# Kernel tuning notes

Hardware: AMD Instinct MI355X
Metric: run time of the kernel (lower is better)

The kernel has to match this reference:

```python
import math
import jax, jax.numpy as jnp
import numpy as np

SM_K = 5

def make_sm_kernel(kernel_size=SM_K, sigma_e=1.2, sigma_i=1.4):
    center = kernel_size // 2
    xx, yy = jnp.meshgrid(jnp.arange(kernel_size, dtype=jnp.float32),
                          jnp.arange(kernel_size, dtype=jnp.float32), indexing='ij')
    xx = xx - center
    yy = yy - center
    g_e = jnp.exp(-(xx ** 2 + yy ** 2) / (2.0 * sigma_e ** 2))
    g_i = jnp.exp(-(xx ** 2 + yy ** 2) / (2.0 * sigma_i ** 2))
    dog = g_e / (2.0 * math.pi * sigma_e ** 2) - g_i / (2.0 * math.pi * sigma_i ** 2)
    return dog / dog[center, center]  # (5,5), normalized so center == 1


def setup_inputs() -> dict:
    key = jax.random.key(0)
    k1, k2 = jax.random.split(key)
    B, Cin, H, W = 16, 64, 128, 128
    Cout, K = 64, 5
    x = jax.random.normal(k1, (B, Cin, H, W), dtype=jnp.float32)
    weight_range = 25.0 / math.sqrt(Cin * K * K)
    weight = weight_range * jnp.abs(jax.random.normal(k2, (Cout, Cin, K, K), dtype=jnp.float32))
    return {"x": x, "weight": weight}


def reference(x, weight):
    PAD = 2
    dn = ('NCHW', 'OIHW', 'NCHW')
    Cout = weight.shape[0]
    K = weight.shape[-1]

    # symmetric_pad -> F.pad reflect
    xp = jnp.pad(x, ((0, 0), (0, 0), (PAD, PAD), (PAD, PAD)), mode='reflect')

    # w = weight.abs(); F.normalize(w, p=2, dim=1): L2 norm over in_channels per (o, kh, kw)
    w = jnp.abs(weight)
    nrm = jnp.sqrt(jnp.sum(w * w, axis=1, keepdims=True))
    w_n = w / jnp.maximum(nrm, 1e-12)

    # cosine similarity: conv with normalized weights / input patch norm
    conv = jax.lax.conv_general_dilated(xp, w_n, (1, 1), 'VALID', dimension_numbers=dn)
    # conv(x^2, ones_like(w)) yields identical values for every output channel;
    # compute once with a single-output-channel ones kernel and broadcast.
    ones_k = jnp.ones((1, x.shape[1], K, K), dtype=x.dtype)
    xsq_sum = jax.lax.conv_general_dilated(xp * xp, ones_k, (1, 1), 'VALID', dimension_numbers=dn)
    y = conv / jnp.sqrt(xsq_sum + 1e-8)  # (B, Cout, H, W)

    # surround modulation: depthwise conv with fixed 5x5 DoG kernel, padding 2
    sm = make_sm_kernel()
    sm_k = jnp.broadcast_to(sm[None, None].astype(y.dtype), (Cout, 1, SM_K, SM_K))
    y = jax.lax.conv_general_dilated(y, sm_k, (1, 1), [(SM_K // 2, SM_K // 2)] * 2,
                                     dimension_numbers=dn, feature_group_count=Cout)
    return y
```

## Files before the change

kernel.cpp:

```cpp
#include <hip/hip_runtime.h>
#include <hip/hip_bf16.h>
#include <math.h>

#define B_   16
#define CIN  64
#define COUT 64
#define H_   128
#define W_   128
#define KK   25
#define HW   (H_ * W_)
#define XT_PLANE ((size_t)B_ * HW * 32)

typedef short  bf16x8 __attribute__((ext_vector_type(8)));
typedef short  s16x4  __attribute__((ext_vector_type(4)));
typedef float  f32x16 __attribute__((ext_vector_type(16)));
typedef float  f32x4  __attribute__((ext_vector_type(4)));
typedef float  f32x2  __attribute__((ext_vector_type(2)));

__device__ __forceinline__ short f2bs(float v) {
    __hip_bfloat16 h = __float2bfloat16(v);
    return *reinterpret_cast<short*>(&h);
}
__device__ __forceinline__ float bs2f(short s) {
    unsigned int u = ((unsigned int)(unsigned short)s) << 16;
    return __uint_as_float(u);
}

__global__ __launch_bounds__(256) void k_prep(const float* __restrict__ x,
                                              const float* __restrict__ w,
                                              short* __restrict__ xt,
                                              float* __restrict__ xsqg,
                                              short* __restrict__ wnb2) {
    const int tid = threadIdx.x;

    if (blockIdx.z == B_) {
        if (blockIdx.x != 0 || blockIdx.y >= COUT) return;
        __shared__ float wl[CIN * KK];
        __shared__ float inv[KK];
        const int o = blockIdx.y;

        for (int idx = tid; idx < CIN * KK; idx += 256)
            wl[idx] = w[(size_t)o * (CIN * KK) + idx];
        __syncthreads();
        if (tid < KK) {
            float s = 0.f;
            #pragma unroll 8
            for (int i = 0; i < CIN; ++i) { float v = wl[i * KK + tid]; s += v * v; }
            inv[tid] = 1.f / fmaxf(sqrtf(s), 1e-12f);
        }
        __syncthreads();
        const int tt = o >> 5, n = o & 31;
        for (int idx = tid; idx < CIN * KK; idx += 256) {
            int ci = idx & 63, kk = idx >> 6;
            int ks = ci >> 4, q = (ci >> 3) & 1, j = ci & 7;
            int l = q * 32 + n;
            wnb2[((size_t)((kk * 4 + ks) * 2 + tt) * 64 + l) * 8 + j] =
                f2bs(fabsf(wl[ci * KK + kk]) * inv[kk]);
        }
        return;
    }

    __shared__ float tile[64][65];
    __shared__ float ps[4][64];
    const int b = blockIdx.z, h = blockIdx.y, w0 = blockIdx.x * 64;

    const float* xb = x + (size_t)b * CIN * HW + h * W_ + w0;
    {
        int wl = tid & 63, c0 = tid >> 6;
        float sq = 0.f;
        #pragma unroll
        for (int cc = 0; cc < 16; ++cc) {
            float v = xb[(size_t)(c0 * 16 + cc) * HW + wl];
            tile[c0 * 16 + cc][wl] = v;
            sq += v * v;
        }
        ps[c0][wl] = sq;
    }
    __syncthreads();

    const size_t pixbase = (size_t)b * HW + h * W_ + w0;
    if (tid < 64)
        xsqg[pixbase + tid] = ps[0][tid] + ps[1][tid] + ps[2][tid] + ps[3][tid];

    {
        int c8 = tid & 7;
        int half = c8 >> 2, sl = c8 & 3;
        short* dp = xt + (size_t)half * XT_PLANE;
        #pragma unroll
        for (int rep = 0; rep < 2; ++rep) {
            int p = (tid >> 3) + rep * 32;
            bf16x8 v;
            #pragma unroll
            for (int j = 0; j < 8; ++j) v[j] = f2bs(tile[c8 * 8 + j][p]);
            *(bf16x8*)&dp[(pixbase + p) * 32 + sl * 8] = v;
        }
    }
}

#define XP 40
#define NR 12
#define NC 36
#define NS (NR * NC)
#define TP 264

__global__ __launch_bounds__(256, 4) void k_conv(const short* __restrict__ xt,
                                                 const float* __restrict__ xsqg,
                                                 const short* __restrict__ wnb2,
                                                 __hip_bfloat16* __restrict__ t) {
    __shared__ short xin[NS * XP];
    __shared__ float s2win[NS];
    __shared__ int   soff[NS];
    __shared__ float xsq[256];

    const int tid  = threadIdx.x;
    const int lane = tid & 63;
    const int wv   = tid >> 6;
    const int n    = lane & 31;
    const int q    = lane >> 5;
    const int b    = blockIdx.z;
    const int h0   = blockIdx.y * 8;
    const int w0   = blockIdx.x * 32;

    const size_t pixbase = (size_t)b * HW;

    for (int s = tid; s < NS; s += 256) {
        int r = s / NC, c = s - r * NC;
        int hh = h0 - 2 + r; hh = hh < 0 ? -hh : (hh > H_ - 1 ? 2 * (H_ - 1) - hh : hh);
        int ww = w0 - 2 + c; ww = ww < 0 ? -ww : (ww > W_ - 1 ? 2 * (W_ - 1) - ww : ww);
        int off = hh * W_ + ww;
        soff[s] = off;
        s2win[s] = xsqg[pixbase + off];
    }
    __syncthreads();

    {
        int hr = tid >> 5, cl = tid & 31;
        float a = 0.f;
        #pragma unroll
        for (int kh = 0; kh < 5; ++kh)
            #pragma unroll
            for (int kw = 0; kw < 5; ++kw)
                a += s2win[(hr + kh) * NC + cl + kw];
        xsq[tid] = a;
    }

    const short* wb = wnb2 + (size_t)lane * 8;

    f32x16 acc00, acc01, acc10, acc11;
    #pragma unroll
    for (int i = 0; i < 16; ++i) { acc00[i] = 0.f; acc01[i] = 0.f; acc10[i] = 0.f; acc11[i] = 0.f; }

    #pragma unroll
    for (int half = 0; half < 2; ++half) {
        const short* xph = xt + (size_t)half * XT_PLANE + pixbase * 32;
        for (int i = tid; i < NS * 4; i += 256) {
            int s = i >> 2, c8 = i & 3;
            *(bf16x8*)&xin[s * 32 + c8 * 8 + (s * 8 & 2047) * 0 + s * (XP - 32)] =
                *(const bf16x8*)&xph[(size_t)soff[s] * 32 + c8 * 8];
        }
        __syncthreads();

        #pragma unroll 5
        for (int kk = 0; kk < KK; ++kk) {
            const int kh = kk / 5, kw = kk % 5;
            const int sp0 = (2 * wv + kh) * NC + n + kw;
            #pragma unroll
            for (int ks2 = 0; ks2 < 2; ++ks2) {
                const int ks = half * 2 + ks2;
                const int ko = ks2 * 16 + q * 8;
                bf16x8 a0 = *(const bf16x8*)&xin[sp0 * XP + ko];
                bf16x8 a1 = *(const bf16x8*)&xin[(sp0 + NC) * XP + ko];
                bf16x8 b0 = *(const bf16x8*)&wb[(size_t)((kk * 4 + ks) * 2 + 0) * 512];
                bf16x8 b1 = *(const bf16x8*)&wb[(size_t)((kk * 4 + ks) * 2 + 1) * 512];
                acc00 = __builtin_amdgcn_mfma_f32_32x32x16_bf16(a0, b0, acc00, 0, 0, 0);
                acc01 = __builtin_amdgcn_mfma_f32_32x32x16_bf16(a0, b1, acc01, 0, 0, 0);
                acc10 = __builtin_amdgcn_mfma_f32_32x32x16_bf16(a1, b0, acc10, 0, 0, 0);
                acc11 = __builtin_amdgcn_mfma_f32_32x32x16_bf16(a1, b1, acc11, 0, 0, 0);
            }
        }
        __syncthreads();
    }

    short* trans = xin;
    const int hrA = 2 * wv, hrB = 2 * wv + 1;
    #pragma unroll
    for (int g4 = 0; g4 < 4; ++g4) {
        int wc0 = 8 * g4 + 4 * q;
        s16x4 v00, v01, v10, v11;
        #pragma unroll
        for (int j = 0; j < 4; ++j) {
            float ia = rsqrtf(xsq[hrA * 32 + wc0 + j] + 1e-8f);
            float ib = rsqrtf(xsq[hrB * 32 + wc0 + j] + 1e-8f);
            v00[j] = f2bs(acc00[4 * g4 + j] * ia);
            v01[j] = f2bs(acc01[4 * g4 + j] * ia);
            v10[j] = f2bs(acc10[4 * g4 + j] * ib);
            v11[j] = f2bs(acc11[4 * g4 + j] * ib);
        }
        *(s16x4*)&trans[n * TP        + hrA * 32 + wc0] = v00;
        *(s16x4*)&trans[(32 + n) * TP + hrA * 32 + wc0] = v01;
        *(s16x4*)&trans[n * TP        + hrB * 32 + wc0] = v10;
        *(s16x4*)&trans[(32 + n) * TP + hrB * 32 + wc0] = v11;
    }
    __syncthreads();

    #pragma unroll
    for (int u = tid; u < 512; u += 256) {
        int oc = u >> 3, hr = u & 7;
        const short* src = &trans[oc * TP + hr * 32];
        __hip_bfloat16* dst = t + ((size_t)(b * COUT + oc) * H_ + h0 + hr) * W_ + w0;
        float4 a0 = *(const float4*)(src);
        float4 a1 = *(const float4*)(src + 8);
        float4 a2 = *(const float4*)(src + 16);
        float4 a3 = *(const float4*)(src + 24);
        *(float4*)(dst)      = a0;
        *(float4*)(dst + 8)  = a1;
        *(float4*)(dst + 16) = a2;
        *(float4*)(dst + 24) = a3;
    }
}

__global__ __launch_bounds__(256) void k_dog(const __hip_bfloat16* __restrict__ t,
                                             float* __restrict__ out) {
    __shared__ float tile[68 * 132];
    __shared__ float sm_s[25];
    const int bo  = blockIdx.y;
    const int h0  = blockIdx.x * 64;
    const int tid = threadIdx.x;

    if (tid < 25) {
        const float se2 = 2.f * 1.2f * 1.2f;
        const float si2 = 2.f * 1.4f * 1.4f;
        const float twopi = 6.28318530717958647692f;
        const float ae = 1.f / (twopi * 1.2f * 1.2f);
        const float ai = 1.f / (twopi * 1.4f * 1.4f);
        const float c0 = ae - ai;
        int dx = tid / 5 - 2, dy = tid % 5 - 2;
        float r2 = (float)(dx * dx + dy * dy);
        sm_s[tid] = (ae * expf(-r2 / se2) - ai * expf(-r2 / si2)) / c0;
    }

    const __hip_bfloat16* tc = t + (size_t)bo * HW;
    for (int idx = tid; idx < 68 * 16; idx += 256) {
        int rr = idx >> 4, g = idx & 15;
        int hh = h0 - 2 + rr;
        float v[8];
        if (hh >= 0 && hh < H_) {
            bf16x8 a = *(const bf16x8*)&tc[hh * W_ + g * 8];
            #pragma unroll
            for (int j = 0; j < 8; ++j) v[j] = bs2f(a[j]);
        } else {
            #pragma unroll
            for (int j = 0; j < 8; ++j) v[j] = 0.f;
        }
        float* dst = &tile[rr * 132 + 2 + g * 8];
        *(f32x2*)(dst)     = (f32x2){v[0], v[1]};
        *(f32x4*)(dst + 2) = (f32x4){v[2], v[3], v[4], v[5]};
        *(f32x2*)(dst + 6) = (f32x2){v[6], v[7]};
    }
    for (int idx = tid; idx < 68 * 4; idx += 256) {
        int rr = idx >> 2, c = idx & 3;
        tile[rr * 132 + (c < 2 ? c : 128 + c)] = 0.f;
    }
    __syncthreads();

    float smr[25];
    #pragma unroll
    for (int kk = 0; kk < 25; ++kk) smr[kk] = sm_s[kk];

    const int cq = tid & 31;
    const int r0 = tid >> 5;
    #pragma unroll
    for (int rr = 0; rr < 8; ++rr) {
        int r = r0 + 8 * rr;
        float s0 = 0.f, s1 = 0.f, s2 = 0.f, s3 = 0.f;
        #pragma unroll
        for (int kh = 0; kh < 5; ++kh) {
            const float* row = &tile[(r + kh) * 132 + cq * 4];
            f32x4 v0 = *(const f32x4*)(row);
            f32x4 v1 = *(const f32x4*)(row + 4);
            float vv[8] = { v0[0], v0[1], v0[2], v0[3], v1[0], v1[1], v1[2], v1[3] };
            #pragma unroll
            for (int kw = 0; kw < 5; ++kw) {
                float cf = smr[kh * 5 + kw];
                s0 += cf * vv[kw];
                s1 += cf * vv[kw + 1];
                s2 += cf * vv[kw + 2];
                s3 += cf * vv[kw + 3];
            }
        }
        float4 o4 = make_float4(s0, s1, s2, s3);
        *(float4*)&out[((size_t)bo * H_ + h0 + r) * W_ + cq * 4] = o4;
    }
}

extern "C" void kernel_launch(void* const* d_in, const int* in_sizes, int n_in,
                              void* d_out, int out_size, void* d_ws, size_t ws_size,
                              hipStream_t stream) {
    const float* x = (const float*)d_in[0];
    const float* w = (const float*)d_in[1];

    __hip_bfloat16* t = (__hip_bfloat16*)d_ws;

    short* xt    = (short*)d_out;
    float* xsqg  = (float*)((char*)d_out + 33554432);
    short* wnb2  = (short*)((char*)d_out + (size_t)67108864 - 204800);

    dim3 gx(W_ / 64, H_, B_ + 1);
    k_prep<<<gx, 256, 0, stream>>>(x, w, xt, xsqg, wnb2);

    dim3 g2(W_ / 32, H_ / 8, B_);
    k_conv<<<g2, 256, 0, stream>>>(xt, xsqg, wnb2, t);

    dim3 g3(H_ / 64, B_ * COUT);
    k_dog<<<g3, 256, 0, stream>>>(t, (float*)d_out);
}
```

Before: 190.8 us.

## Tile intermediate layout by width strip and vectorize prep input loads

Measured after the change: 189.9 us. Within noise of the previous version (-0.5%).

```diff
diff --git a/kernel.cpp b/kernel.cpp
--- a/kernel.cpp
+++ b/kernel.cpp
@@ -10,6 +10,7 @@
 #define KK   25
 #define HW   (H_ * W_)
 #define XT_PLANE ((size_t)B_ * HW * 32)
+#define WTS ((size_t)COUT * H_ * 32)
 
 typedef short  bf16x8 __attribute__((ext_vector_type(8)));
 typedef short  s16x4  __attribute__((ext_vector_type(4)));
@@ -61,27 +62,22 @@
     }
 
     __shared__ float tile[64][65];
-    __shared__ float ps[4][64];
+    __shared__ float ps[8][64];
     const int b = blockIdx.z, h = blockIdx.y, w0 = blockIdx.x * 64;
 
     const float* xb = x + (size_t)b * CIN * HW + h * W_ + w0;
     {
-        int wl = tid & 63, c0 = tid >> 6;
-        float sq = 0.f;
-        #pragma unroll
-        for (int cc = 0; cc < 16; ++cc) {
-            float v = xb[(size_t)(c0 * 16 + cc) * HW + wl];
-            tile[c0 * 16 + cc][wl] = v;
-            sq += v * v;
-        }
-        ps[c0][wl] = sq;
+        int c4 = tid & 15, g = tid >> 4;
+        #pragma unroll
+        for (int k = 0; k < 4; ++k) {
+            int ci = g * 4 + k;
+            *(f32x4*)&tile[ci][c4 * 4] =
+                *(const f32x4*)&xb[(size_t)ci * HW + c4 * 4];
+        }
     }
     __syncthreads();
 
     const size_t pixbase = (size_t)b * HW + h * W_ + w0;
-    if (tid < 64)
-        xsqg[pixbase + tid] = ps[0][tid] + ps[1][tid] + ps[2][tid] + ps[3][tid];
-
     {
         int c8 = tid & 7;
         int half = c8 >> 2, sl = c8 & 3;
@@ -89,11 +85,23 @@
         #pragma unroll
         for (int rep = 0; rep < 2; ++rep) {
             int p = (tid >> 3) + rep * 32;
-            bf16x8 v;
-            #pragma unroll
-            for (int j = 0; j < 8; ++j) v[j] = f2bs(tile[c8 * 8 + j][p]);
+            bf16x8 v; float sq = 0.f;
+            #pragma unroll
+            for (int j = 0; j < 8; ++j) {
+                float f = tile[c8 * 8 + j][p];
+                sq += f * f;
+                v[j] = f2bs(f);
+            }
+            ps[c8][p] = sq;
             *(bf16x8*)&dp[(pixbase + p) * 32 + sl * 8] = v;
         }
+    }
+    __syncthreads();
+    if (tid < 64) {
+        float a = 0.f;
+        #pragma unroll
+        for (int c8 = 0; c8 < 8; ++c8) a += ps[c8][tid];
+        xsqg[pixbase + tid] = a;
     }
 }
 
@@ -106,7 +114,7 @@
 __global__ __launch_bounds__(256, 4) void k_conv(const short* __restrict__ xt,
                                                  const float* __restrict__ xsqg,
                                                  const short* __restrict__ wnb2,
-                                                 __hip_bfloat16* __restrict__ t) {
+                                                 short* __restrict__ t2) {
     __shared__ short xin[NS * XP];
     __shared__ float s2win[NS];
     __shared__ int   soff[NS];
@@ -119,7 +127,8 @@
     const int q    = lane >> 5;
     const int b    = blockIdx.z;
     const int h0   = blockIdx.y * 8;
-    const int w0   = blockIdx.x * 32;
+    const int wt   = blockIdx.x;
+    const int w0   = wt * 32;
 
     const size_t pixbase = (size_t)b * HW;
 
@@ -155,7 +164,7 @@
         const short* xph = xt + (size_t)half * XT_PLANE + pixbase * 32;
         for (int i = tid; i < NS * 4; i += 256) {
             int s = i >> 2, c8 = i & 3;
-            *(bf16x8*)&xin[s * 32 + c8 * 8 + (s * 8 & 2047) * 0 + s * (XP - 32)] =
+            *(bf16x8*)&xin[s * XP + c8 * 8] =
                 *(const bf16x8*)&xph[(size_t)soff[s] * 32 + c8 * 8];
         }
         __syncthreads();
@@ -203,11 +212,12 @@
     }
     __syncthreads();
 
+    short* tbase = t2 + ((size_t)(b * 4 + wt) * COUT) * (H_ * 32);
     #pragma unroll
     for (int u = tid; u < 512; u += 256) {
         int oc = u >> 3, hr = u & 7;
         const short* src = &trans[oc * TP + hr * 32];
-        __hip_bfloat16* dst = t + ((size_t)(b * COUT + oc) * H_ + h0 + hr) * W_ + w0;
+        short* dst = tbase + ((size_t)oc * H_ + h0 + hr) * 32;
         float4 a0 = *(const float4*)(src);
         float4 a1 = *(const float4*)(src + 8);
         float4 a2 = *(const float4*)(src + 16);
@@ -219,7 +229,7 @@
     }
 }
 
-__global__ __launch_bounds__(256) void k_dog(const __hip_bfloat16* __restrict__ t,
+__global__ __launch_bounds__(256) void k_dog(const short* __restrict__ t2,
                                              float* __restrict__ out) {
     __shared__ float tile[68 * 132];
     __shared__ float sm_s[25];
@@ -239,13 +249,15 @@
         sm_s[tid] = (ae * expf(-r2 / se2) - ai * expf(-r2 / si2)) / c0;
     }
 
-    const __hip_bfloat16* tc = t + (size_t)bo * HW;
+    const int bb = bo >> 6, oc = bo & 63;
+    const short* base = t2 + ((size_t)(bb * 4) * COUT + oc) * (H_ * 32);
     for (int idx = tid; idx < 68 * 16; idx += 256) {
         int rr = idx >> 4, g = idx & 15;
         int hh = h0 - 2 + rr;
         float v[8];
         if (hh >= 0 && hh < H_) {
-            bf16x8 a = *(const bf16x8*)&tc[hh * W_ + g * 8];
+            int wtile = g >> 2, c = g & 3;
+            bf16x8 a = *(const bf16x8*)&base[(size_t)wtile * WTS + (size_t)hh * 32 + c * 8];
             #pragma unroll
             for (int j = 0; j < 8; ++j) v[j] = bs2f(a[j]);
         } else {
@@ -299,7 +311,7 @@
     const float* x = (const float*)d_in[0];
     const float* w = (const float*)d_in[1];
 
-    __hip_bfloat16* t = (__hip_bfloat16*)d_ws;
+    short* t2 = (short*)d_ws;
 
     short* xt    = (short*)d_out;
     float* xsqg  = (float*)((char*)d_out + 33554432);
@@ -309,8 +321,8 @@
     k_prep<<<gx, 256, 0, stream>>>(x, w, xt, xsqg, wnb2);
 
     dim3 g2(W_ / 32, H_ / 8, B_);
-    k_conv<<<g2, 256, 0, stream>>>(xt, xsqg, wnb2, t);
+    k_conv<<<g2, 256, 0, stream>>>(xt, xsqg, wnb2, t2);
 
     dim3 g3(H_ / 64, B_ * COUT);
-    k_dog<<<g3, 256, 0, stream>>>(t, (float*)d_out);
-}
+    k_dog<<<g3, 256, 0, stream>>>(t2, (float*)d_out);
+}
```
